# Kernel optimization log

Measured on AMD Instinct MI355X. Metric: run time of the kernel, lower is better.

Reference implementation:

```python
import jax, jax.numpy as jnp
import numpy as np
from itertools import combinations_with_replacement

IN_FEATURES = 128
ORDER = 3
BIAS = True
WEIGHT_DIVISOR = 100.0
BATCH = 256


def _make_comb_idx():
    n_feat = IN_FEATURES + (1 if BIAS else 0)  # 129
    idx = np.array(list(combinations_with_replacement(range(n_feat), ORDER)), dtype=np.int32)
    return jnp.asarray(idx)  # [num_combinations, ORDER] = [366145, 3]


def setup_inputs() -> dict:
    key = jax.random.key(0)
    kx, kw = jax.random.split(key)
    x = jax.random.normal(kx, (BATCH, IN_FEATURES), dtype=jnp.float32)
    comb_idx = _make_comb_idx()
    num_weights = comb_idx.shape[0]
    weight = jax.random.uniform(kw, (num_weights,), dtype=jnp.float32) / WEIGHT_DIVISOR
    return {"x": x, "weight": weight, "comb_idx": comb_idx}


def reference(x, weight, comb_idx):
    # Prepend bias column of ones: xb [B, in_features+1]
    ones = jnp.ones((x.shape[0], 1), dtype=x.dtype)
    xb = jnp.concatenate([ones, x], axis=1)
    # Gather per-combination features: [B, num_combinations, ORDER]
    gathered = xb[:, comb_idx]
    # Monomial products: [B, num_combinations]
    colx = jnp.prod(gathered, axis=2)
    # Weighted sum -> [B, 1]; activation is identity
    return colx @ weight[:, None]
```

## Files before the change

### kernel.cpp

```cpp
#include <hip/hip_runtime.h>


#define NF      129
#define NCOMB   366145
#define NPAIR   8385
#define NT      4
#define NCHUNK  132
#define NKS     4

typedef short bf16x8 __attribute__((ext_vector_type(8)));
typedef float f32x4  __attribute__((ext_vector_type(4)));

union i4b8 { int4 i; bf16x8 b; };

static __device__ inline unsigned bfpack2(float lo, float hi) {
    union { float f; unsigned u; } a, b; a.f = lo; b.f = hi;
    return ((b.u + 0x8000u) & 0xffff0000u) | ((a.u + 0x8000u) >> 16);
}

static __device__ inline void dpair(int p, int& i0, int& i1) {
    int t = (int)((259.0f - sqrtf((float)(67081 - 8 * p))) * 0.5f);
    t = t < 0 ? 0 : (t > 128 ? 128 : t);
    while (t < 128 && ((t + 1) * (258 - t)) / 2 <= p) ++t;
    while (t > 0   && (t * (259 - t)) / 2      >  p) --t;
    i0 = t; i1 = t + (p - (t * (259 - t)) / 2);
}

static __device__ inline int mbase(int i0, int i1) {
    const int n0 = NF - i0, n1 = NF - i1;
    return NCOMB - (n0 * (n0 + 1) * (n0 + 2)) / 6
                 + ((n0 * (n0 + 1)) >> 1) - ((n1 * (n1 + 1)) >> 1);
}

__global__ __launch_bounds__(256, 3) void honu_fused(const float* __restrict__ x,
                                                     const float* __restrict__ w,
                                                     float* __restrict__ out) {
    __shared__ float  xf[64 * NF];
    __shared__ bf16x8 wls[NT * NKS * 64];
    __shared__ int4   dec[64];

    const int tid  = threadIdx.x;
    const int lane = tid & 63;
    const int wv   = tid >> 6;
    const int bx   = blockIdx.x;
    const int by   = blockIdx.y;

    {
        const int r = tid >> 2, q = tid & 3;
        const float4* xr = (const float4*)(x + (size_t)(by * 64 + r) * 128);
        #pragma unroll
        for (int t = 0; t < 8; ++t) {
            const int c4 = q + 4 * t;
            const float4 v = xr[c4];
            float* d = &xf[r * NF + 1 + 4 * c4];
            d[0] = v.x; d[1] = v.y; d[2] = v.z; d[3] = v.w;
        }
        if (tid < 64) xf[tid * NF] = 1.0f;
    }

    if (tid < 64) {
        const int p = bx * 64 + tid;
        int i0 = 0, i1 = 200, mb = 0; unsigned wl = 0;
        if (p < NPAIR) {
            dpair(p, i0, i1);
            mb = mbase(i0, i1);
            union { float f; unsigned u; } c; c.f = w[mb + 128 - i1];
            wl = c.u;
        }
        dec[tid] = make_int4(i0 | (i1 << 16), mb, (int)wl, 0);
    }
    __syncthreads();

    #pragma unroll
    for (int it = 0; it < 4; ++it) {
        const int item = tid + it * 256;
        const int pl = item >> 4, r = item & 15;
        const int4 pd = dec[pl];
        const int i1 = pd.x >> 16;
        const int mb = pd.y;
        const int k0 = r * 8;
        int4 vout = make_int4(0, 0, 0, 0);
        if (k0 + 7 >= i1) {
            float f[8];
            #pragma unroll
            for (int j = 0; j < 8; ++j) {
                const int k = k0 + j;
                int off = k - i1; off = off < 0 ? 0 : off;
                const float t = w[mb + off];
                f[j] = (k >= i1) ? t : 0.0f;
            }
            vout.x = (int)bfpack2(f[0], f[1]);
            vout.y = (int)bfpack2(f[2], f[3]);
            vout.z = (int)bfpack2(f[4], f[5]);
            vout.w = (int)bfpack2(f[6], f[7]);
        }
        const int nt = pl >> 4, s = r >> 2;
        const int slane = ((r & 3) << 4) | (pl & 15);
        ((int4*)wls)[(nt * NKS + s) * 64 + slane] = vout;
    }

    const int am = wv * 16 + (lane & 15);
    const int aq = (lane >> 4) * 8;
    const float* xa = &xf[am * NF + aq];
    bf16x8 a[NKS];
    #pragma unroll
    for (int s = 0; s < NKS; ++s) {
        const float* p = xa + s * 32;
        i4b8 av;
        av.i.x = (int)bfpack2(p[0], p[1]);
        av.i.y = (int)bfpack2(p[2], p[3]);
        av.i.z = (int)bfpack2(p[4], p[5]);
        av.i.w = (int)bfpack2(p[6], p[7]);
        a[s] = av.b;
    }
    __syncthreads();

    const int lr0 = wv * 16 + (lane >> 4) * 4;
    const float* r0 = &xf[lr0 * NF];
    float o0 = 0.f, o1 = 0.f, o2 = 0.f, o3 = 0.f;

    #pragma unroll
    for (int nt = 0; nt < NT; ++nt) {
        f32x4 acc = {0.f, 0.f, 0.f, 0.f};
        #pragma unroll
        for (int s = 0; s < NKS; ++s)
            acc = __builtin_amdgcn_mfma_f32_16x16x32_bf16(
                      a[s], wls[(nt * NKS + s) * 64 + lane], acc, 0, 0, 0);

        const int4 pd = dec[nt * 16 + (lane & 15)];
        const int i0 = pd.x & 0xffff;
        int i1 = pd.x >> 16; if (i1 > 128) i1 = 0;
        union { int i; float f; } wc; wc.i = pd.z;
        const float wl = wc.f;
        o0 = fmaf(acc[0] + r0[128]          * wl, r0[i0]          * r0[i1],          o0);
        o1 = fmaf(acc[1] + r0[NF + 128]     * wl, r0[NF + i0]     * r0[NF + i1],     o1);
        o2 = fmaf(acc[2] + r0[2 * NF + 128] * wl, r0[2 * NF + i0] * r0[2 * NF + i1], o2);
        o3 = fmaf(acc[3] + r0[3 * NF + 128] * wl, r0[3 * NF + i0] * r0[3 * NF + i1], o3);
    }

    #pragma unroll
    for (int msk = 1; msk < 16; msk <<= 1) {
        o0 += __shfl_xor(o0, msk);
        o1 += __shfl_xor(o1, msk);
        o2 += __shfl_xor(o2, msk);
        o3 += __shfl_xor(o3, msk);
    }
    if ((lane & 15) == 0) {
        float* po = out + by * 64 + lr0;
        atomicAdd(po + 0, o0);
        atomicAdd(po + 1, o1);
        atomicAdd(po + 2, o2);
        atomicAdd(po + 3, o3);
    }
}

extern "C" void kernel_launch(void* const* d_in, const int* in_sizes, int n_in,
                              void* d_out, int out_size, void* d_ws, size_t ws_size,
                              hipStream_t stream) {
    const float* x      = (const float*)d_in[0];
    const float* weight = (const float*)d_in[1];
    float* out = (float*)d_out;

    honu_fused<<<dim3(NCHUNK, 4), 256, 0, stream>>>(x, weight, out);
}
```

Before: 76.82 us.

## Stage block's weight range into LDS as bf16 slab before scatter

Each block now computes the contiguous weight range covering its 64 pairs, loads it with coalesced reads, converts it to bf16 and stores it in a shared slab that aliases the x buffer. The scatter into MFMA B-fragments then reads from this slab instead of making strided, duplicated global loads. x is held in registers and written to LDS after the slab is consumed, which costs two extra barriers. The slab length must fit in the aliased x buffer, and the sizing relies on that holding.

```diff
diff --git a/kernel.cpp b/kernel.cpp
--- a/kernel.cpp
+++ b/kernel.cpp
@@ -10,8 +10,6 @@
 
 typedef short bf16x8 __attribute__((ext_vector_type(8)));
 typedef float f32x4  __attribute__((ext_vector_type(4)));
-
-union i4b8 { int4 i; bf16x8 b; };
 
 static __device__ inline unsigned bfpack2(float lo, float hi) {
     union { float f; unsigned u; } a, b; a.f = lo; b.f = hi;
@@ -35,9 +33,11 @@
 __global__ __launch_bounds__(256, 3) void honu_fused(const float* __restrict__ x,
                                                      const float* __restrict__ w,
                                                      float* __restrict__ out) {
-    __shared__ float  xf[64 * NF];
+    __shared__ char   uA[64 * NF * 4];
     __shared__ bf16x8 wls[NT * NKS * 64];
     __shared__ int4   dec[64];
+    float*          xf   = (float*)uA;
+    unsigned short* slab = (unsigned short*)uA;
 
     const int tid  = threadIdx.x;
     const int lane = tid & 63;
@@ -45,29 +45,38 @@
     const int bx   = blockIdx.x;
     const int by   = blockIdx.y;
 
+    const int p0 = bx * 64;
+    int a0, a1; dpair(p0, a0, a1);
+    const int mstart = mbase(a0, a1);
+    int mend = NCOMB;
+    if (p0 + 64 < NPAIR) { int b0, b1; dpair(p0 + 64, b0, b1); mend = mbase(b0, b1); }
+    const int L = mend - mstart;
+
+    float4 xreg[8];
     {
         const int r = tid >> 2, q = tid & 3;
-        const float4* xr = (const float4*)(x + (size_t)(by * 64 + r) * 128);
+        const float4* xrp = (const float4*)(x + (size_t)(by * 64 + r) * 128);
         #pragma unroll
-        for (int t = 0; t < 8; ++t) {
-            const int c4 = q + 4 * t;
-            const float4 v = xr[c4];
-            float* d = &xf[r * NF + 1 + 4 * c4];
-            d[0] = v.x; d[1] = v.y; d[2] = v.z; d[3] = v.w;
-        }
-        if (tid < 64) xf[tid * NF] = 1.0f;
+        for (int t = 0; t < 8; ++t) xreg[t] = xrp[q + 4 * t];
     }
 
     if (tid < 64) {
-        const int p = bx * 64 + tid;
-        int i0 = 0, i1 = 200, mb = 0; unsigned wl = 0;
+        const int p = p0 + tid;
+        int i0 = 0, i1 = 200, mb = 0, bo = 0; unsigned wl = 0;
         if (p < NPAIR) {
             dpair(p, i0, i1);
             mb = mbase(i0, i1);
+            bo = mb - mstart - i1;
             union { float f; unsigned u; } c; c.f = w[mb + 128 - i1];
             wl = c.u;
         }
-        dec[tid] = make_int4(i0 | (i1 << 16), mb, (int)wl, 0);
+        dec[tid] = make_int4(i0 | (i1 << 16), mb, (int)wl, bo);
+    }
+
+    for (int i = tid * 2; i < L; i += 512) {
+        const float lo = w[mstart + i];
+        const float hi = (i + 1 < L) ? w[mstart + i + 1] : 0.0f;
+        ((unsigned*)slab)[i >> 1] = bfpack2(lo, hi);
     }
     __syncthreads();
 
@@ -77,27 +86,40 @@
         const int pl = item >> 4, r = item & 15;
         const int4 pd = dec[pl];
         const int i1 = pd.x >> 16;
-        const int mb = pd.y;
+        const int bo = pd.w;
         const int k0 = r * 8;
         int4 vout = make_int4(0, 0, 0, 0);
         if (k0 + 7 >= i1) {
-            float f[8];
+            unsigned sv[8];
             #pragma unroll
             for (int j = 0; j < 8; ++j) {
                 const int k = k0 + j;
-                int off = k - i1; off = off < 0 ? 0 : off;
-                const float t = w[mb + off];
-                f[j] = (k >= i1) ? t : 0.0f;
+                int ad = bo + k; ad = ad < 0 ? 0 : ad;
+                const unsigned t = slab[ad];
+                sv[j] = (k >= i1) ? t : 0u;
             }
-            vout.x = (int)bfpack2(f[0], f[1]);
-            vout.y = (int)bfpack2(f[2], f[3]);
-            vout.z = (int)bfpack2(f[4], f[5]);
-            vout.w = (int)bfpack2(f[6], f[7]);
+            vout.x = (int)(sv[0] | (sv[1] << 16));
+            vout.y = (int)(sv[2] | (sv[3] << 16));
+            vout.z = (int)(sv[4] | (sv[5] << 16));
+            vout.w = (int)(sv[6] | (sv[7] << 16));
         }
         const int nt = pl >> 4, s = r >> 2;
         const int slane = ((r & 3) << 4) | (pl & 15);
         ((int4*)wls)[(nt * NKS + s) * 64 + slane] = vout;
     }
+    __syncthreads();
+
+    {
+        const int r = tid >> 2, q = tid & 3;
+        #pragma unroll
+        for (int t = 0; t < 8; ++t) {
+            const int c4 = q + 4 * t;
+            float* d = &xf[r * NF + 1 + 4 * c4];
+            d[0] = xreg[t].x; d[1] = xreg[t].y; d[2] = xreg[t].z; d[3] = xreg[t].w;
+        }
+        if (tid < 64) xf[tid * NF] = 1.0f;
+    }
+    __syncthreads();
 
     const int am = wv * 16 + (lane & 15);
     const int aq = (lane >> 4) * 8;
@@ -106,14 +128,13 @@
     #pragma unroll
     for (int s = 0; s < NKS; ++s) {
         const float* p = xa + s * 32;
-        i4b8 av;
+        union { int4 i; bf16x8 b; } av;
         av.i.x = (int)bfpack2(p[0], p[1]);
         av.i.y = (int)bfpack2(p[2], p[3]);
         av.i.z = (int)bfpack2(p[4], p[5]);
         av.i.w = (int)bfpack2(p[6], p[7]);
         a[s] = av.b;
     }
-    __syncthreads();
 
     const int lr0 = wv * 16 + (lane >> 4) * 4;
     const float* r0 = &xf[lr0 * NF];
```

Result: no change. 78.07 us (+1.6%).
